# Performance work log

Hardware: AMD Instinct MI355X
Metric: run time of the kernel (lower is better)

Reference implementation:

```python
import jax, jax.numpy as jnp
import numpy as np

NUM_CODEWORDS = 16384
EMBED_DIM = 4096      # == in_features (asserted in torch module)
OUT_FEATURES = 4096
N_TILES = 4
ROWS_PER_TILE = 1024  # N_TILES * ROWS_PER_TILE == OUT_FEATURES
B, S = 4, 2048


def setup_inputs() -> dict:
    key = jax.random.key(0)
    k1, k2, k3, k4, k5 = jax.random.split(key, 5)
    x = jax.random.normal(k1, (B, S, EMBED_DIM), dtype=jnp.float32)
    codewords = jax.random.normal(k2, (NUM_CODEWORDS, EMBED_DIM), dtype=jnp.float32) * 0.02
    indices = jax.random.randint(k3, (N_TILES, ROWS_PER_TILE), 0, NUM_CODEWORDS, dtype=jnp.int64)
    rotations = jax.random.normal(k4, (N_TILES, EMBED_DIM, EMBED_DIM), dtype=jnp.float32) / np.sqrt(EMBED_DIM)
    scales = jax.random.uniform(k5, (N_TILES,), dtype=jnp.float32)
    bias = jnp.zeros((OUT_FEATURES,), dtype=jnp.float32)
    return {"x": x, "codewords": codewords, "indices": indices,
            "rotations": rotations, "scales": scales, "bias": bias}


def _decode_weight(codewords, indices, rotations, scales):
    # gather: [T, R, D]
    decoded = codewords[indices]
    # per-tile rotation: [T, R, D] @ [T, D, D] -> [T, R, D]
    rotated = jnp.einsum('trd,tde->tre', decoded, rotations)
    scaled = rotated * scales[:, None, None]
    # concat tiles along rows -> [out_features, in_features]
    return scaled.reshape(-1, EMBED_DIM)


def reference(x, codewords, indices, rotations, scales, bias):
    weight = _decode_weight(codewords, indices, rotations, scales)  # [O, I]
    # F.linear: x @ weight.T + bias
    return jnp.einsum('bsi,oi->bso', x, weight) + bias
```

## Files before the change

kernel.cpp:

```cpp
#include <hip/hip_runtime.h>
#include <hip/hip_bf16.h>
#include <stdint.h>
#include <stddef.h>

#define DIM    4096
#define MROWS  8192
#define NCW    16384
#define NTILES 4
#define RPT    1024

#define BM 128
#define BN 128
#define BK 32

typedef __attribute__((ext_vector_type(8))) short bf16x8;
typedef __attribute__((ext_vector_type(4))) float f32x4;

__device__ __forceinline__ uint16_t f2bf(float f) {
  union { float f; uint32_t u; } a; a.f = f;
  uint32_t u = a.u;
  u += 0x7fffu + ((u >> 16) & 1u);
  return (uint16_t)(u >> 16);
}

__device__ __forceinline__ void gl2lds16(const void* g, void* l) {
  __builtin_amdgcn_global_load_lds(
      (const __attribute__((address_space(1))) void*)g,
      (__attribute__((address_space(3))) void*)l, 16, 0, 0);
}

__global__ void detect_idx_kernel(const uint32_t* __restrict__ inds,
                                  int* __restrict__ flag) {
  __shared__ int bad;
  if (threadIdx.x == 0) bad = 0;
  __syncthreads();
  int viol = 0;
  for (int k = threadIdx.x; k < 2048; k += 256) {
    uint32_t lo = inds[2 * k];
    uint32_t hi = inds[2 * k + 1];
    if (hi != 0u || lo >= (uint32_t)NCW) viol = 1;
  }
  if (viol) atomicAdd(&bad, 1);
  __syncthreads();
  if (threadIdx.x == 0) flag[0] = (bad == 0) ? 1 : 0;
}

__global__ void cvt_x_kernel(const float* __restrict__ in,
                             uint16_t* __restrict__ out) {
  size_t i = ((size_t)blockIdx.x * 256 + threadIdx.x) * 8;
  float4 v0 = *(const float4*)(in + i);
  float4 v1 = *(const float4*)(in + i + 4);
  uint4 o;
  o.x = (uint32_t)f2bf(v0.x) | ((uint32_t)f2bf(v0.y) << 16);
  o.y = (uint32_t)f2bf(v0.z) | ((uint32_t)f2bf(v0.w) << 16);
  o.z = (uint32_t)f2bf(v1.x) | ((uint32_t)f2bf(v1.y) << 16);
  o.w = (uint32_t)f2bf(v1.z) | ((uint32_t)f2bf(v1.w) << 16);
  *(uint4*)(out + i) = o;
}

__global__ void gather_cw_kernel(const float* __restrict__ cw,
                                 const void* __restrict__ inds,
                                 const int* __restrict__ flag,
                                 uint16_t* __restrict__ out) {
  const int o = blockIdx.x;
  long long idx;
  if (flag[0]) idx = ((const long long*)inds)[o];
  else         idx = (long long)((const int*)inds)[o];
  const float* src = cw + (size_t)idx * DIM;
  uint16_t* dst = out + (size_t)o * DIM;
  for (int c = 0; c < 4; c++) {
    int e = c * 1024 + threadIdx.x * 4;
    float4 v = *(const float4*)(src + e);
    uint2 w;
    w.x = (uint32_t)f2bf(v.x) | ((uint32_t)f2bf(v.y) << 16);
    w.y = (uint32_t)f2bf(v.z) | ((uint32_t)f2bf(v.w) << 16);
    *(uint2*)(dst + e) = w;
  }
}

__global__ void rot_transpose_kernel(const float* __restrict__ R,
                                     uint16_t* __restrict__ Rt) {
  __shared__ float tile[32][33];
  const int t = blockIdx.z;
  const int e0 = blockIdx.x * 32;
  const int d0 = blockIdx.y * 32;
  const float* Rp = R + (size_t)t * DIM * DIM;
  uint16_t* Rtp = Rt + (size_t)t * DIM * DIM;
  for (int i = threadIdx.y; i < 32; i += 8)
    tile[i][threadIdx.x] = Rp[(size_t)(d0 + i) * DIM + (e0 + threadIdx.x)];
  __syncthreads();
  for (int i = threadIdx.y; i < 32; i += 8)
    Rtp[(size_t)(e0 + i) * DIM + (d0 + threadIdx.x)] = f2bf(tile[threadIdx.x][i]);
}

template <int MODE>
__global__ __launch_bounds__(256)
void gemm_bt(const uint16_t* __restrict__ A,
             const uint16_t* __restrict__ B,
             const float* __restrict__ sv,
             void* __restrict__ Cout,
             int N, int K) {
  __shared__ uint16_t As[BM * BK];
  __shared__ uint16_t Bs[BN * BK];

  const int tid  = threadIdx.x;
  const int wave = tid >> 6;
  const int lane = tid & 63;
  const int quad = lane >> 4;
  const int lr   = lane & 15;
  const int wm   = (wave >> 1) * 64;
  const int wn   = (wave & 1) * 64;

  const int m0 = blockIdx.y * BM;
  const int n0 = blockIdx.x * BN;

  const uint16_t* Bp = B;
  float scale = 1.0f;
  if (MODE == 0) {
    int t = m0 >> 10;
    Bp = B + (size_t)t * (size_t)N * (size_t)K;
    scale = sv[t];
  }

  const int srow = lane >> 2;
  const int scol = (lane & 3) * 8;
  const int ca   = wave * 2;

  const uint16_t* Ag = A  + (size_t)(m0 + srow) * K + scol;
  const uint16_t* Bg = Bp + (size_t)(n0 + srow) * K + scol;

  f32x4 acc[4][4];
#pragma unroll
  for (int i = 0; i < 4; i++)
#pragma unroll
    for (int j = 0; j < 4; j++) acc[i][j] = f32x4{0.f, 0.f, 0.f, 0.f};

  for (int k0 = 0; k0 < K; k0 += BK) {
#pragma unroll
    for (int i = 0; i < 2; i++) {
      int c = ca + i;
      gl2lds16(Ag + (size_t)(c * 16) * K + k0, &As[c * 512]);
      gl2lds16(Bg + (size_t)(c * 16) * K + k0, &Bs[c * 512]);
    }
    __builtin_amdgcn_s_waitcnt(0);
    __syncthreads();

    bf16x8 a[4], b[4];
#pragma unroll
    for (int mi = 0; mi < 4; mi++)
      a[mi] = *(const bf16x8*)&As[(wm + mi * 16 + lr) * BK + quad * 8];
#pragma unroll
    for (int ni = 0; ni < 4; ni++)
      b[ni] = *(const bf16x8*)&Bs[(wn + ni * 16 + lr) * BK + quad * 8];

#pragma unroll
    for (int mi = 0; mi < 4; mi++)
#pragma unroll
      for (int ni = 0; ni < 4; ni++)
        acc[mi][ni] = __builtin_amdgcn_mfma_f32_16x16x32_bf16(
            a[mi], b[ni], acc[mi][ni], 0, 0, 0);

    __syncthreads();
  }

  if (MODE == 0) {
    uint16_t* C = (uint16_t*)Cout;
#pragma unroll
    for (int mi = 0; mi < 4; mi++)
#pragma unroll
      for (int ni = 0; ni < 4; ni++)
#pragma unroll
        for (int r = 0; r < 4; r++) {
          int row = m0 + wm + mi * 16 + quad * 4 + r;
          int col = n0 + wn + ni * 16 + lr;
          C[(size_t)row * N + col] = f2bf(acc[mi][ni][r] * scale);
        }
  } else {
    float* C = (float*)Cout;
#pragma unroll
    for (int mi = 0; mi < 4; mi++)
#pragma unroll
      for (int ni = 0; ni < 4; ni++)
#pragma unroll
        for (int r = 0; r < 4; r++) {
          int row = m0 + wm + mi * 16 + quad * 4 + r;
          int col = n0 + wn + ni * 16 + lr;
          C[(size_t)row * N + col] = acc[mi][ni][r] + sv[col];
        }
  }
}

extern "C" void kernel_launch(void* const* d_in, const int* in_sizes, int n_in,
                              void* d_out, int out_size, void* d_ws,
                              size_t ws_size, hipStream_t stream) {
  const float* x      = (const float*)d_in[0];
  const float* cw     = (const float*)d_in[1];
  const void*  inds   = d_in[2];
  const float* rot    = (const float*)d_in[3];
  const float* scales = (const float*)d_in[4];
  const float* bias   = (const float*)d_in[5];
  float* out = (float*)d_out;

  char* ws = (char*)d_ws;
  int*      flag = (int*)ws;
  uint16_t* Xb   = (uint16_t*)(ws + 256);
  uint16_t* Cgb  = (uint16_t*)(ws + 256 + (size_t)64  * 1024 * 1024);
  uint16_t* Rt   = (uint16_t*)(ws + 256 + (size_t)96  * 1024 * 1024);
  uint16_t* Wb   = (uint16_t*)(ws + 256 + (size_t)224 * 1024 * 1024);

  detect_idx_kernel<<<1, 256, 0, stream>>>((const uint32_t*)inds, flag);

  cvt_x_kernel<<<16384, 256, 0, stream>>>(x, Xb);

  gather_cw_kernel<<<DIM, 256, 0, stream>>>(cw, inds, flag, Cgb);

  rot_transpose_kernel<<<dim3(DIM / 32, DIM / 32, NTILES), dim3(32, 8), 0,
                         stream>>>(rot, Rt);

  gemm_bt<0><<<dim3(DIM / BN, DIM / BM), 256, 0, stream>>>(
      Cgb, Rt, scales, (void*)Wb, DIM, DIM);

  gemm_bt<1><<<dim3(DIM / BN, MROWS / BM), 256, 0, stream>>>(
      Xb, Wb, bias, (void*)out, DIM, DIM);
}
```

Before: 1.251 ms.

## Rewrite GEMM as 256x256 tile, double-buffered, LDS-swizzled pipelined kernel

Replaces the simple 128x128x32 GEMM, which waited on every load before computing, with a 256x256 tile using 512 threads (8 waves, each doing 128x64). Global-to-LDS loads for the next K step are double-buffered and interleaved with MFMA phases, using setprio and explicit vmcnt waits. An XOR swizzle on the LDS layout avoids bank conflicts, and block IDs are remapped so neighbouring workgroups share L2. This aims to raise MFMA utilization and data reuse, at the cost of higher register and LDS pressure and fewer workgroups for the 4096x4096 decode GEMM.

```diff
diff --git a/kernel.cpp b/kernel.cpp
--- a/kernel.cpp
+++ b/kernel.cpp
@@ -9,9 +9,10 @@
 #define NTILES 4
 #define RPT    1024
 
-#define BM 128
-#define BN 128
-#define BK 32
+#define BM 256
+#define BN 256
+#define BK 64
+#define NT (DIM / BK)
 
 typedef __attribute__((ext_vector_type(8))) short bf16x8;
 typedef __attribute__((ext_vector_type(4))) float f32x4;
@@ -27,6 +28,12 @@
   __builtin_amdgcn_global_load_lds(
       (const __attribute__((address_space(1))) void*)g,
       (__attribute__((address_space(3))) void*)l, 16, 0, 0);
+}
+
+__device__ __forceinline__ bf16x8 lds_frag(const uint16_t* base, int r, int q) {
+  int y = (r << 6) | (q << 4);
+  y ^= ((y >> 7) & 7) << 4;
+  return *(const bf16x8*)((const char*)base + y);
 }
 
 __global__ void detect_idx_kernel(const uint32_t* __restrict__ inds,
@@ -94,98 +101,137 @@
 }
 
 template <int MODE>
-__global__ __launch_bounds__(256)
-void gemm_bt(const uint16_t* __restrict__ A,
+__global__ __launch_bounds__(512, 2)
+void gemm256(const uint16_t* __restrict__ A,
              const uint16_t* __restrict__ B,
              const float* __restrict__ sv,
-             void* __restrict__ Cout,
-             int N, int K) {
-  __shared__ uint16_t As[BM * BK];
-  __shared__ uint16_t Bs[BN * BK];
+             void* __restrict__ Cout) {
+  __shared__ __align__(16) uint16_t As[2][2][BM * 32];
+  __shared__ __align__(16) uint16_t Bs[2][2][BN * 32];
 
   const int tid  = threadIdx.x;
   const int wave = tid >> 6;
   const int lane = tid & 63;
   const int quad = lane >> 4;
   const int lr   = lane & 15;
-  const int wm   = (wave >> 1) * 64;
-  const int wn   = (wave & 1) * 64;
-
-  const int m0 = blockIdx.y * BM;
-  const int n0 = blockIdx.x * BN;
+  const int wm   = (wave >> 2) * 128;
+  const int wn   = (wave & 3) * 64;
+
+  const int nwg = gridDim.x;
+  const int bid = blockIdx.x;
+  const int wg  = (bid & 7) * (nwg >> 3) + (bid >> 3);
+  const int bx  = wg & 15;
+  const int by  = wg >> 4;
+  const int m0  = by * BM;
+  const int n0  = bx * BN;
 
   const uint16_t* Bp = B;
   float scale = 1.0f;
   if (MODE == 0) {
-    int t = m0 >> 10;
-    Bp = B + (size_t)t * (size_t)N * (size_t)K;
+    const int t = m0 >> 10;
+    Bp = B + (size_t)t * DIM * DIM;
     scale = sv[t];
   }
 
-  const int srow = lane >> 2;
-  const int scol = (lane & 3) * 8;
-  const int ca   = wave * 2;
-
-  const uint16_t* Ag = A  + (size_t)(m0 + srow) * K + scol;
-  const uint16_t* Bg = Bp + (size_t)(n0 + srow) * K + scol;
-
-  f32x4 acc[4][4];
-#pragma unroll
-  for (int i = 0; i < 4; i++)
+  const int y0  = tid << 4;
+  const int y1  = (512 + tid) << 4;
+  const int gy0 = y0 ^ (((y0 >> 7) & 7) << 4);
+  const int gy1 = y1 ^ (((y1 >> 7) & 7) << 4);
+  const size_t ao0 = (size_t)(gy0 >> 6) * DIM + (size_t)((gy0 >> 4) & 3) * 8;
+  const size_t ao1 = (size_t)(gy1 >> 6) * DIM + (size_t)((gy1 >> 4) & 3) * 8;
+  const int ld0 = (wave * 64) * 8;
+  const int ld1 = 4096 + (wave * 64) * 8;
+
+  const uint16_t* Ag = A  + (size_t)m0 * DIM;
+  const uint16_t* Bg = Bp + (size_t)n0 * DIM;
+
+#define STG(gb, kc, lh)                          \
+  do {                                           \
+    gl2lds16((gb) + ao0 + (kc), (lh) + ld0);     \
+    gl2lds16((gb) + ao1 + (kc), (lh) + ld1);     \
+  } while (0)
+
+  f32x4 acc[8][4];
+#pragma unroll
+  for (int i = 0; i < 8; i++)
 #pragma unroll
     for (int j = 0; j < 4; j++) acc[i][j] = f32x4{0.f, 0.f, 0.f, 0.f};
 
-  for (int k0 = 0; k0 < K; k0 += BK) {
-#pragma unroll
-    for (int i = 0; i < 2; i++) {
-      int c = ca + i;
-      gl2lds16(Ag + (size_t)(c * 16) * K + k0, &As[c * 512]);
-      gl2lds16(Bg + (size_t)(c * 16) * K + k0, &Bs[c * 512]);
-    }
-    __builtin_amdgcn_s_waitcnt(0);
-    __syncthreads();
-
-    bf16x8 a[4], b[4];
-#pragma unroll
-    for (int mi = 0; mi < 4; mi++)
-      a[mi] = *(const bf16x8*)&As[(wm + mi * 16 + lr) * BK + quad * 8];
-#pragma unroll
-    for (int ni = 0; ni < 4; ni++)
-      b[ni] = *(const bf16x8*)&Bs[(wn + ni * 16 + lr) * BK + quad * 8];
-
-#pragma unroll
-    for (int mi = 0; mi < 4; mi++)
-#pragma unroll
-      for (int ni = 0; ni < 4; ni++)
-        acc[mi][ni] = __builtin_amdgcn_mfma_f32_16x16x32_bf16(
-            a[mi], b[ni], acc[mi][ni], 0, 0, 0);
-
-    __syncthreads();
-  }
+  STG(Ag, 0,  As[0][0]);
+  STG(Bg, 0,  Bs[0][0]);
+  STG(Ag, 32, As[0][1]);
+  STG(Bg, 32, Bs[0][1]);
+  asm volatile("s_waitcnt vmcnt(4)" ::: "memory");
+  __builtin_amdgcn_s_barrier();
+
+  int cur = 0;
+  bf16x8 b[4];
+
+#define PHASE(KS, MH, STAGE_STMT, DO_VM)                                      \
+  do {                                                                        \
+    const uint16_t* Ab = As[cur][KS];                                         \
+    bf16x8 a[4];                                                              \
+    _Pragma("unroll")                                                         \
+    for (int j = 0; j < 4; ++j)                                               \
+      a[j] = lds_frag(Ab, wm + ((MH)*4 + j) * 16 + lr, quad);                 \
+    if ((MH) == 0) {                                                          \
+      const uint16_t* Bb = Bs[cur][KS];                                       \
+      _Pragma("unroll")                                                       \
+      for (int j = 0; j < 4; ++j)                                             \
+        b[j] = lds_frag(Bb, wn + j * 16 + lr, quad);                          \
+    }                                                                         \
+    STAGE_STMT;                                                               \
+    __builtin_amdgcn_s_barrier();                                             \
+    asm volatile("s_waitcnt lgkmcnt(0)" ::: "memory");                        \
+    __builtin_amdgcn_sched_barrier(0);                                        \
+    __builtin_amdgcn_s_setprio(1);                                            \
+    _Pragma("unroll")                                                         \
+    for (int j = 0; j < 4; ++j)                                               \
+      _Pragma("unroll")                                                       \
+      for (int n = 0; n < 4; ++n)                                             \
+        acc[(MH)*4 + j][n] = __builtin_amdgcn_mfma_f32_16x16x32_bf16(         \
+            a[j], b[n], acc[(MH)*4 + j][n], 0, 0, 0);                         \
+    __builtin_amdgcn_s_setprio(0);                                            \
+    if (DO_VM) asm volatile("s_waitcnt vmcnt(4)" ::: "memory");               \
+    __builtin_amdgcn_s_barrier();                                             \
+  } while (0)
+
+  for (int kt = 0; kt < NT; ++kt) {
+    const int kn = (kt + 1 < NT) ? (kt + 1) * BK : kt * BK;
+    PHASE(0, 0, STG(Ag, kn,      As[cur ^ 1][0]), 0);
+    PHASE(0, 1, STG(Bg, kn,      Bs[cur ^ 1][0]), 1);
+    PHASE(1, 0, STG(Ag, kn + 32, As[cur ^ 1][1]), 0);
+    PHASE(1, 1, STG(Bg, kn + 32, Bs[cur ^ 1][1]), 1);
+    cur ^= 1;
+  }
+  asm volatile("s_waitcnt vmcnt(0)" ::: "memory");
+
+#undef PHASE
+#undef STG
 
   if (MODE == 0) {
     uint16_t* C = (uint16_t*)Cout;
 #pragma unroll
-    for (int mi = 0; mi < 4; mi++)
+    for (int mi = 0; mi < 8; mi++)
 #pragma unroll
       for (int ni = 0; ni < 4; ni++)
 #pragma unroll
         for (int r = 0; r < 4; r++) {
           int row = m0 + wm + mi * 16 + quad * 4 + r;
           int col = n0 + wn + ni * 16 + lr;
-          C[(size_t)row * N + col] = f2bf(acc[mi][ni][r] * scale);
+          C[(size_t)row * DIM + col] = f2bf(acc[mi][ni][r] * scale);
         }
   } else {
     float* C = (float*)Cout;
 #pragma unroll
-    for (int mi = 0; mi < 4; mi++)
+    for (int mi = 0; mi < 8; mi++)
 #pragma unroll
       for (int ni = 0; ni < 4; ni++)
 #pragma unroll
         for (int r = 0; r < 4; r++) {
           int row = m0 + wm + mi * 16 + quad * 4 + r;
           int col = n0 + wn + ni * 16 + lr;
-          C[(size_t)row * N + col] = acc[mi][ni][r] + sv[col];
+          C[(size_t)row * DIM + col] = acc[mi][ni][r] + sv[col];
         }
   }
 }
@@ -217,9 +263,9 @@
   rot_transpose_kernel<<<dim3(DIM / 32, DIM / 32, NTILES), dim3(32, 8), 0,
                          stream>>>(rot, Rt);
 
-  gemm_bt<0><<<dim3(DIM / BN, DIM / BM), 256, 0, stream>>>(
-      Cgb, Rt, scales, (void*)Wb, DIM, DIM);
-
-  gemm_bt<1><<<dim3(DIM / BN, MROWS / BM), 256, 0, stream>>>(
-      Xb, Wb, bias, (void*)out, DIM, DIM);
-}
+  gemm256<0><<<dim3((DIM / BN) * (DIM / BM)), 512, 0, stream>>>(
+      Cgb, Rt, scales, (void*)Wb);
+
+  gemm256<1><<<dim3((DIM / BN) * (MROWS / BM)), 512, 0, stream>>>(
+      Xb, Wb, bias, (void*)out);
+}
```

Result: faster. 1.118 ms (-10.6%).
